# Optimization experiments

Measured on AMD Instinct MI355X. Metric: run time of the kernel, lower is better.

Reference implementation:

```python
import jax, jax.numpy as jnp
import numpy as np

B = 65536
QUERY_DIM = 1024
CROSS_DIM = 1024
HEADS = 16
DIM_HEAD = 64
INNER = HEADS * DIM_HEAD  # 1024
SCALE = DIM_HEAD ** -0.5


def setup_inputs() -> dict:
    key = jax.random.key(0)
    ks = jax.random.split(key, 7)
    s_in = 1.0 / np.sqrt(QUERY_DIM)
    s_c = 1.0 / np.sqrt(CROSS_DIM)
    s_o = 1.0 / np.sqrt(INNER)
    return {
        "latent": jax.random.normal(ks[0], (B, QUERY_DIM), jnp.float32),
        "cond_latent": jax.random.normal(ks[1], (B, CROSS_DIM), jnp.float32),
        "Wq": jax.random.normal(ks[2], (INNER, QUERY_DIM), jnp.float32) * s_in,
        "Wk": jax.random.normal(ks[3], (INNER, CROSS_DIM), jnp.float32) * s_c,
        "Wv": jax.random.normal(ks[4], (INNER, CROSS_DIM), jnp.float32) * s_c,
        "Wout": jax.random.normal(ks[5], (QUERY_DIM, INNER), jnp.float32) * s_o,
        "bout": jax.random.normal(ks[6], (QUERY_DIM,), jnp.float32) * s_o,
    }


def reference(latent, cond_latent, Wq, Wk, Wv, Wout, bout):
    # projections: [B, inner] -> [B, heads, dim_head]
    Q = (latent @ Wq.T).reshape(B, HEADS, DIM_HEAD)
    K = (cond_latent @ Wk.T).reshape(B, HEADS, DIM_HEAD)
    V = (cond_latent @ Wv.T).reshape(B, HEADS, DIM_HEAD)
    # attention across the heads axis: scores [B, heads, heads]
    scores = jnp.einsum("bhd,bgd->bhg", Q, K) * SCALE
    probs = jax.nn.softmax(scores, axis=-1)
    feats = jnp.einsum("bhg,bgd->bhd", probs, V).reshape(B, INNER)
    return feats @ Wout.T + bout
```

## Files before the change

kernel.cpp:

```cpp
#include <hip/hip_runtime.h>
#include <hip/hip_bf16.h>

#define NB    65536
#define KDIM  1024
#define NDIM  1024

#define BM 256
#define BN 256
#define BK 64
#define NT (KDIM / BK)

typedef float f32x4 __attribute__((ext_vector_type(4)));
typedef short short8 __attribute__((ext_vector_type(8)));
typedef unsigned short ushort8v __attribute__((ext_vector_type(8)));

static __device__ __forceinline__ unsigned short f2bf(float f) {
    union { float f; unsigned u; } v; v.f = f;
    unsigned r = v.u + 0x7FFFu + ((v.u >> 16) & 1u);
    return (unsigned short)(r >> 16);
}
static __device__ __forceinline__ float bf2f(unsigned short h) {
    union { unsigned u; float f; } v; v.u = ((unsigned)h) << 16;
    return v.f;
}

static __device__ __forceinline__ void gload16(const unsigned short* g, unsigned short* l) {
    __builtin_amdgcn_global_load_lds(
        (const __attribute__((address_space(1))) unsigned int*)g,
        (__attribute__((address_space(3))) unsigned int*)l, 16, 0, 0);
}

__global__ __launch_bounds__(256) void f32_to_bf16_k(
    const float* __restrict__ s, unsigned short* __restrict__ d, int n4)
{
    const int stride = gridDim.x * 256;
    for (int i = blockIdx.x * 256 + threadIdx.x; i < n4; i += stride) {
        float4 v = reinterpret_cast<const float4*>(s)[i];
        ushort4 o;
        o.x = f2bf(v.x); o.y = f2bf(v.y); o.z = f2bf(v.z); o.w = f2bf(v.w);
        reinterpret_cast<ushort4*>(d)[i] = o;
    }
}

template<int OUT_F32>
__global__ __launch_bounds__(512, 2) void gemm256(
    const unsigned short* __restrict__ Ap, const unsigned short* __restrict__ Wp,
    const float* __restrict__ bias, void* __restrict__ Cptr)
{
    constexpr int N = NDIM;
    constexpr int GN = NDIM / BN;
    __shared__ alignas(16) unsigned short lds[2][2][32][512];

    const int t    = threadIdx.x;
    const int lane = t & 63;
    const int wid  = t >> 6;
    const int wm   = wid >> 2;
    const int wn   = wid & 3;

    const int nwg  = gridDim.x;
    const int cpx  = nwg >> 3;
    const int orig = blockIdx.x;
    const int wgid = (orig & 7) * cpx + (orig >> 3);
    const int bn0  = (wgid & (GN - 1)) * BN;
    const int bm0  = (wgid / GN) * BM;

    const size_t aoff = (size_t)(lane & 15) * KDIM + (lane >> 4) * 8;

#define LDA_(BUF, MI, KS) \
    (*reinterpret_cast<const short8*>(&lds[BUF][0][(wm * 8 + (MI)) * 2 + (KS)][lane * 8]))
#define LDB_(BUF, NI, KS) \
    (*reinterpret_cast<const short8*>(&lds[BUF][1][(wn * 4 + (NI)) * 2 + (KS)][lane * 8]))

#define STAGE_(TAU, SLOT, AB, KS) do {                                          \
        int _tc = (TAU) < NT ? (TAU) : NT - 1;   \
        const unsigned short* _b = (AB) ? Wp : Ap;                              \
        int _r0 = (AB) ? bn0 : bm0;                                             \
        _Pragma("unroll")                                                       \
        for (int _j = 0; _j < 2; ++_j) {                                        \
            int _f = wid * 2 + _j;                                              \
            gload16(_b + (size_t)(_r0 + _f * 16) * KDIM + _tc * BK + (KS) * 32 + aoff, \
                    &lds[SLOT][AB][_f * 2 + (KS)][0]);                          \
        }                                                                       \
    } while (0)

#define PHASE_SYNC() do {                                                       \
        asm volatile("s_waitcnt vmcnt(8)" ::: "memory");                        \
        __builtin_amdgcn_s_barrier();                                           \
        asm volatile("s_waitcnt lgkmcnt(0)" ::: "memory");                      \
        __builtin_amdgcn_sched_barrier(0);                                      \
    } while (0)

#define MFMA_LO() do { _Pragma("unroll")                                        \
    for (int mi = 0; mi < 8; ++mi) {                                            \
        acc[mi][0] = __builtin_amdgcn_mfma_f32_16x16x32_bf16(af[mi], bq0, acc[mi][0], 0, 0, 0); \
        acc[mi][1] = __builtin_amdgcn_mfma_f32_16x16x32_bf16(af[mi], bq1, acc[mi][1], 0, 0, 0); \
    } } while (0)
#define MFMA_HI() do { _Pragma("unroll")                                        \
    for (int mi = 0; mi < 8; ++mi) {                                            \
        acc[mi][2] = __builtin_amdgcn_mfma_f32_16x16x32_bf16(af[mi], bq2, acc[mi][2], 0, 0, 0); \
        acc[mi][3] = __builtin_amdgcn_mfma_f32_16x16x32_bf16(af[mi], bq3, acc[mi][3], 0, 0, 0); \
    } } while (0)

#define GROUP_(BUF, OBUF, TT) do {                                              \
                                                      \
        _Pragma("unroll")                                                       \
        for (int mi = 0; mi < 8; ++mi) af[mi] = LDA_(BUF, mi, 0);               \
        bq0 = LDB_(BUF, 0, 0); bq1 = LDB_(BUF, 1, 0);                           \
        STAGE_((TT) + 1, OBUF, 0, 1);                                           \
        PHASE_SYNC();                                                           \
        __builtin_amdgcn_s_setprio(1); MFMA_LO(); __builtin_amdgcn_s_setprio(0);\
        __builtin_amdgcn_s_barrier();                                           \
                                                      \
        bq2 = LDB_(BUF, 2, 0); bq3 = LDB_(BUF, 3, 0);                           \
        STAGE_((TT) + 1, OBUF, 1, 1);                                           \
        PHASE_SYNC();                                                           \
        __builtin_amdgcn_s_setprio(1); MFMA_HI(); __builtin_amdgcn_s_setprio(0);\
        __builtin_amdgcn_s_barrier();                                           \
                                                      \
        _Pragma("unroll")                                                       \
        for (int mi = 0; mi < 8; ++mi) af[mi] = LDA_(BUF, mi, 1);               \
        bq0 = LDB_(BUF, 0, 1); bq1 = LDB_(BUF, 1, 1);                           \
        STAGE_((TT) + 2, BUF, 0, 0);                                            \
        PHASE_SYNC();                                                           \
        __builtin_amdgcn_s_setprio(1); MFMA_LO(); __builtin_amdgcn_s_setprio(0);\
        __builtin_amdgcn_s_barrier();                                           \
                                                      \
        bq2 = LDB_(BUF, 2, 1); bq3 = LDB_(BUF, 3, 1);                           \
        STAGE_((TT) + 2, BUF, 1, 0);                                            \
        PHASE_SYNC();                                                           \
        __builtin_amdgcn_s_setprio(1); MFMA_HI(); __builtin_amdgcn_s_setprio(0);\
        __builtin_amdgcn_s_barrier();                                           \
    } while (0)

    f32x4 acc[8][4];
#pragma unroll
    for (int mi = 0; mi < 8; ++mi)
#pragma unroll
        for (int ni = 0; ni < 4; ++ni)
            acc[mi][ni] = (f32x4){0.f, 0.f, 0.f, 0.f};

    short8 af[8], bq0, bq1, bq2, bq3;

    STAGE_(0, 0, 0, 0); STAGE_(0, 0, 1, 0);
    STAGE_(0, 0, 0, 1); STAGE_(0, 0, 1, 1);
    STAGE_(1, 1, 0, 0); STAGE_(1, 1, 1, 0);
    asm volatile("s_waitcnt vmcnt(8)" ::: "memory");
    __builtin_amdgcn_s_barrier();

#pragma unroll 1
    for (int tt = 0; tt < NT; tt += 2) {
        GROUP_(0, 1, tt);
        GROUP_(1, 0, tt + 1);
    }

    const int crow = (lane >> 4) * 4;
    const int ccol = lane & 15;
    if (OUT_F32) {
        float* Cf = (float*)Cptr;
        float bv[4];
#pragma unroll
        for (int ni = 0; ni < 4; ++ni)
            bv[ni] = bias[bn0 + wn * 64 + ni * 16 + ccol];
#pragma unroll
        for (int mi = 0; mi < 8; ++mi)
#pragma unroll
            for (int ni = 0; ni < 4; ++ni) {
                size_t base = (size_t)(bm0 + wm * 128 + mi * 16 + crow) * N
                            + (bn0 + wn * 64 + ni * 16 + ccol);
#pragma unroll
                for (int r = 0; r < 4; ++r)
                    Cf[base + (size_t)r * N] = acc[mi][ni][r] + bv[ni];
            }
    } else {
        unsigned short* Cb = (unsigned short*)Cptr;
#pragma unroll
        for (int mi = 0; mi < 8; ++mi)
#pragma unroll
            for (int ni = 0; ni < 4; ++ni) {
                size_t base = (size_t)(bm0 + wm * 128 + mi * 16 + crow) * N
                            + (bn0 + wn * 64 + ni * 16 + ccol);
#pragma unroll
                for (int r = 0; r < 4; ++r)
                    Cb[base + (size_t)r * N] = f2bf(acc[mi][ni][r]);
            }
    }
#undef LDA_
#undef LDB_
#undef STAGE_
#undef PHASE_SYNC
#undef MFMA_LO
#undef MFMA_HI
#undef GROUP_
}

__global__ __launch_bounds__(256) void attn_k(
    const unsigned short* __restrict__ Qb, const unsigned short* __restrict__ Kb,
    const unsigned short* __restrict__ Vb, unsigned short* __restrict__ Fb)
{
    __shared__ alignas(16) unsigned short KL[4][1024];
    __shared__ alignas(16) unsigned short VL[4][1024];
    const int t = threadIdx.x;
    const int lane = t & 63;
    const int wid = t >> 6;
    const size_t row = (size_t)blockIdx.x * 4 + wid;
    const size_t base = row * 1024;
    const int off = lane * 16;

    ushort8v q0 = *reinterpret_cast<const ushort8v*>(&Qb[base + off]);
    ushort8v q1 = *reinterpret_cast<const ushort8v*>(&Qb[base + off + 8]);
    float qf[16];
#pragma unroll
    for (int j = 0; j < 8; ++j) { qf[j] = bf2f(q0[j]); qf[8 + j] = bf2f(q1[j]); }

    *reinterpret_cast<ushort8v*>(&KL[wid][off])     = *reinterpret_cast<const ushort8v*>(&Kb[base + off]);
    *reinterpret_cast<ushort8v*>(&KL[wid][off + 8]) = *reinterpret_cast<const ushort8v*>(&Kb[base + off + 8]);
    *reinterpret_cast<ushort8v*>(&VL[wid][off])     = *reinterpret_cast<const ushort8v*>(&Vb[base + off]);
    *reinterpret_cast<ushort8v*>(&VL[wid][off + 8]) = *reinterpret_cast<const ushort8v*>(&Vb[base + off + 8]);
    __syncthreads();

    const int sub = lane & 3;
    float s[16];
#pragma unroll
    for (int g = 0; g < 16; ++g) {
        const ushort8v k0 = *reinterpret_cast<const ushort8v*>(&KL[wid][g * 64 + sub * 16]);
        const ushort8v k1 = *reinterpret_cast<const ushort8v*>(&KL[wid][g * 64 + sub * 16 + 8]);
        float acc = 0.f;
#pragma unroll
        for (int j = 0; j < 8; ++j)
            acc += qf[j] * bf2f(k0[j]) + qf[8 + j] * bf2f(k1[j]);
        s[g] = acc;
    }
#pragma unroll
    for (int m = 1; m <= 2; m <<= 1)
#pragma unroll
        for (int g = 0; g < 16; ++g)
            s[g] += __shfl_xor(s[g], m, 64);

    float mx = s[0];
#pragma unroll
    for (int g = 1; g < 16; ++g) mx = fmaxf(mx, s[g]);
    float p[16], denom = 0.f;
#pragma unroll
    for (int g = 0; g < 16; ++g) {
        p[g] = __expf((s[g] - mx) * 0.125f);
        denom += p[g];
    }
    float inv = 1.f / denom;

    float f[16];
#pragma unroll
    for (int j = 0; j < 16; ++j) f[j] = 0.f;
#pragma unroll
    for (int g = 0; g < 16; ++g) {
        float pg = p[g] * inv;
        const ushort8v v0 = *reinterpret_cast<const ushort8v*>(&VL[wid][g * 64 + sub * 16]);
        const ushort8v v1 = *reinterpret_cast<const ushort8v*>(&VL[wid][g * 64 + sub * 16 + 8]);
#pragma unroll
        for (int j = 0; j < 8; ++j) {
            f[j]     += pg * bf2f(v0[j]);
            f[8 + j] += pg * bf2f(v1[j]);
        }
    }
    ushort8v o0, o1;
#pragma unroll
    for (int j = 0; j < 8; ++j) { o0[j] = f2bf(f[j]); o1[j] = f2bf(f[8 + j]); }
    *reinterpret_cast<ushort8v*>(&Fb[base + off])     = o0;
    *reinterpret_cast<ushort8v*>(&Fb[base + off + 8]) = o1;
}

extern "C" void kernel_launch(void* const* d_in, const int* in_sizes, int n_in,
                              void* d_out, int out_size, void* d_ws, size_t ws_size,
                              hipStream_t stream)
{
    (void)in_sizes; (void)n_in; (void)out_size; (void)ws_size;
    const float* latent = (const float*)d_in[0];
    const float* cond   = (const float*)d_in[1];
    const float* Wq     = (const float*)d_in[2];
    const float* Wk     = (const float*)d_in[3];
    const float* Wv     = (const float*)d_in[4];
    const float* Wout   = (const float*)d_in[5];
    const float* bout   = (const float*)d_in[6];
    float* out = (float*)d_out;

    char* ws = (char*)d_ws;
    const size_t MB = 1ull << 20;
    unsigned short* wqb = (unsigned short*)(ws + 0 * MB);
    unsigned short* wkb = (unsigned short*)(ws + 2 * MB);
    unsigned short* wvb = (unsigned short*)(ws + 4 * MB);
    unsigned short* wob = (unsigned short*)(ws + 6 * MB);
    unsigned short* Qb  = (unsigned short*)(ws + 8 * MB);
    unsigned short* Kbf = (unsigned short*)(ws + 8 * MB + 128 * MB);
    unsigned short* Vbf = (unsigned short*)(ws + 8 * MB + 256 * MB);
    unsigned short* Lb  = (unsigned short*)(ws + 8 * MB + 384 * MB);
    unsigned short* Cb  = (unsigned short*)(ws + 8 * MB + 512 * MB);

    const int wn4 = (KDIM * NDIM) / 4;
    f32_to_bf16_k<<<1024, 256, 0, stream>>>(Wq,   wqb, wn4);
    f32_to_bf16_k<<<1024, 256, 0, stream>>>(Wk,   wkb, wn4);
    f32_to_bf16_k<<<1024, 256, 0, stream>>>(Wv,   wvb, wn4);
    f32_to_bf16_k<<<1024, 256, 0, stream>>>(Wout, wob, wn4);

    const int an4 = (NB * KDIM) / 4;
    f32_to_bf16_k<<<4096, 256, 0, stream>>>(latent, Lb, an4);
    f32_to_bf16_k<<<4096, 256, 0, stream>>>(cond,   Cb, an4);

    const int nblk = (NB / BM) * (NDIM / BN);
    gemm256<0><<<nblk, 512, 0, stream>>>(Lb, wqb, nullptr, Qb);
    gemm256<0><<<nblk, 512, 0, stream>>>(Cb, wkb, nullptr, Kbf);
    gemm256<0><<<nblk, 512, 0, stream>>>(Cb, wvb, nullptr, Vbf);

    attn_k<<<NB / 4, 256, 0, stream>>>(Qb, Kbf, Vbf, Qb);

    gemm256<1><<<nblk, 512, 0, stream>>>(Qb, wob, bout, out);
}
```

Measured before the change: 1.009 ms.

## Split GEMM phases by M-halves and relax per-phase memory waits

The bf16 GEMM inner loop now splits each k-slice into two M-halves, each covering all four N fragments, instead of splitting it into two N-halves covering all eight M fragments. B fragments are loaded once per k-slice. The explicit lgkmcnt(0) wait and the sched_barrier are dropped, and the vmcnt wait before the barrier now happens every other phase. The aim is to cut stall points and give the compiler more freedom to overlap LDS reads with MFMAs. In exchange, correctness now depends on the compiler-inserted waits and on fewer global-load waits being enough, and a final vmcnt(0) is added before the epilogue.

```diff
diff --git a/kernel.cpp b/kernel.cpp
--- a/kernel.cpp
+++ b/kernel.cpp
@@ -66,13 +66,18 @@
 
     const size_t aoff = (size_t)(lane & 15) * KDIM + (lane >> 4) * 8;
 
+#define FENCE_ asm volatile("" ::: "memory")
+#define BAR_   do { FENCE_; __builtin_amdgcn_s_barrier(); FENCE_; } while (0)
+#define VMBAR_ do { asm volatile("s_waitcnt vmcnt(8)" ::: "memory");            \
+                    __builtin_amdgcn_s_barrier(); FENCE_; } while (0)
+
 #define LDA_(BUF, MI, KS) \
     (*reinterpret_cast<const short8*>(&lds[BUF][0][(wm * 8 + (MI)) * 2 + (KS)][lane * 8]))
 #define LDB_(BUF, NI, KS) \
     (*reinterpret_cast<const short8*>(&lds[BUF][1][(wn * 4 + (NI)) * 2 + (KS)][lane * 8]))
 
 #define STAGE_(TAU, SLOT, AB, KS) do {                                          \
-        int _tc = (TAU) < NT ? (TAU) : NT - 1;   \
+        int _tc = (TAU) < NT ? (TAU) : NT - 1;    \
         const unsigned short* _b = (AB) ? Wp : Ap;                              \
         int _r0 = (AB) ? bn0 : bm0;                                             \
         _Pragma("unroll")                                                       \
@@ -83,53 +88,47 @@
         }                                                                       \
     } while (0)
 
-#define PHASE_SYNC() do {                                                       \
-        asm volatile("s_waitcnt vmcnt(8)" ::: "memory");                        \
-        __builtin_amdgcn_s_barrier();                                           \
-        asm volatile("s_waitcnt lgkmcnt(0)" ::: "memory");                      \
-        __builtin_amdgcn_sched_barrier(0);                                      \
-    } while (0)
-
-#define MFMA_LO() do { _Pragma("unroll")                                        \
-    for (int mi = 0; mi < 8; ++mi) {                                            \
-        acc[mi][0] = __builtin_amdgcn_mfma_f32_16x16x32_bf16(af[mi], bq0, acc[mi][0], 0, 0, 0); \
-        acc[mi][1] = __builtin_amdgcn_mfma_f32_16x16x32_bf16(af[mi], bq1, acc[mi][1], 0, 0, 0); \
+#define MFMA_(ACCB, AF) do { _Pragma("unroll")                                  \
+    for (int mi = 0; mi < 4; ++mi) {                                            \
+        acc[(ACCB) + mi][0] = __builtin_amdgcn_mfma_f32_16x16x32_bf16(AF[mi], bq0, acc[(ACCB) + mi][0], 0, 0, 0); \
+        acc[(ACCB) + mi][1] = __builtin_amdgcn_mfma_f32_16x16x32_bf16(AF[mi], bq1, acc[(ACCB) + mi][1], 0, 0, 0); \
+        acc[(ACCB) + mi][2] = __builtin_amdgcn_mfma_f32_16x16x32_bf16(AF[mi], bq2, acc[(ACCB) + mi][2], 0, 0, 0); \
+        acc[(ACCB) + mi][3] = __builtin_amdgcn_mfma_f32_16x16x32_bf16(AF[mi], bq3, acc[(ACCB) + mi][3], 0, 0, 0); \
     } } while (0)
-#define MFMA_HI() do { _Pragma("unroll")                                        \
-    for (int mi = 0; mi < 8; ++mi) {                                            \
-        acc[mi][2] = __builtin_amdgcn_mfma_f32_16x16x32_bf16(af[mi], bq2, acc[mi][2], 0, 0, 0); \
-        acc[mi][3] = __builtin_amdgcn_mfma_f32_16x16x32_bf16(af[mi], bq3, acc[mi][3], 0, 0, 0); \
-    } } while (0)
 
 #define GROUP_(BUF, OBUF, TT) do {                                              \
-                                                      \
-        _Pragma("unroll")                                                       \
-        for (int mi = 0; mi < 8; ++mi) af[mi] = LDA_(BUF, mi, 0);               \
+                                                   \
+        _Pragma("unroll")                                                       \
+        for (int mi = 0; mi < 4; ++mi) afA[mi] = LDA_(BUF, mi, 0);              \
         bq0 = LDB_(BUF, 0, 0); bq1 = LDB_(BUF, 1, 0);                           \
+        bq2 = LDB_(BUF, 2, 0); bq3 = LDB_(BUF, 3, 0);                           \
         STAGE_((TT) + 1, OBUF, 0, 1);                                           \
-        PHASE_SYNC();                                                           \
-        __builtin_amdgcn_s_setprio(1); MFMA_LO(); __builtin_amdgcn_s_setprio(0);\
-        __builtin_amdgcn_s_barrier();                                           \
-                                                      \
-        bq2 = LDB_(BUF, 2, 0); bq3 = LDB_(BUF, 3, 0);                           \
+        BAR_;                                                                   \
+        __builtin_amdgcn_s_setprio(1); MFMA_(0, afA); __builtin_amdgcn_s_setprio(0); \
+        BAR_;                                                                   \
+                                                   \
+        _Pragma("unroll")                                                       \
+        for (int mi = 0; mi < 4; ++mi) afB[mi] = LDA_(BUF, 4 + mi, 0);          \
         STAGE_((TT) + 1, OBUF, 1, 1);                                           \
-        PHASE_SYNC();                                                           \
-        __builtin_amdgcn_s_setprio(1); MFMA_HI(); __builtin_amdgcn_s_setprio(0);\
-        __builtin_amdgcn_s_barrier();                                           \
-                                                      \
-        _Pragma("unroll")                                                       \
-        for (int mi = 0; mi < 8; ++mi) af[mi] = LDA_(BUF, mi, 1);               \
+        VMBAR_;                                                                 \
+        __builtin_amdgcn_s_setprio(1); MFMA_(4, afB); __builtin_amdgcn_s_setprio(0); \
+        BAR_;                                                                   \
+                                                   \
+        _Pragma("unroll")                                                       \
+        for (int mi = 0; mi < 4; ++mi) afA[mi] = LDA_(BUF, mi, 1);              \
         bq0 = LDB_(BUF, 0, 1); bq1 = LDB_(BUF, 1, 1);                           \
+        bq2 = LDB_(BUF, 2, 1); bq3 = LDB_(BUF, 3, 1);                           \
         STAGE_((TT) + 2, BUF, 0, 0);                                            \
-        PHASE_SYNC();                                                           \
-        __builtin_amdgcn_s_setprio(1); MFMA_LO(); __builtin_amdgcn_s_setprio(0);\
-        __builtin_amdgcn_s_barrier();                                           \
-                                                      \
-        bq2 = LDB_(BUF, 2, 1); bq3 = LDB_(BUF, 3, 1);                           \
+        BAR_;                                                                   \
+        __builtin_amdgcn_s_setprio(1); MFMA_(0, afA); __builtin_amdgcn_s_setprio(0); \
+        BAR_;                                                                   \
+                                                   \
+        _Pragma("unroll")                                                       \
+        for (int mi = 0; mi < 4; ++mi) afB[mi] = LDA_(BUF, 4 + mi, 1);          \
         STAGE_((TT) + 2, BUF, 1, 0);                                            \
-        PHASE_SYNC();                                                           \
-        __builtin_amdgcn_s_setprio(1); MFMA_HI(); __builtin_amdgcn_s_setprio(0);\
-        __builtin_amdgcn_s_barrier();                                           \
+        VMBAR_;                                                                 \
+        __builtin_amdgcn_s_setprio(1); MFMA_(4, afB); __builtin_amdgcn_s_setprio(0); \
+        BAR_;                                                                   \
     } while (0)
 
     f32x4 acc[8][4];
@@ -139,19 +138,20 @@
         for (int ni = 0; ni < 4; ++ni)
             acc[mi][ni] = (f32x4){0.f, 0.f, 0.f, 0.f};
 
-    short8 af[8], bq0, bq1, bq2, bq3;
+    short8 afA[4], afB[4], bq0, bq1, bq2, bq3;
 
     STAGE_(0, 0, 0, 0); STAGE_(0, 0, 1, 0);
     STAGE_(0, 0, 0, 1); STAGE_(0, 0, 1, 1);
     STAGE_(1, 1, 0, 0); STAGE_(1, 1, 1, 0);
-    asm volatile("s_waitcnt vmcnt(8)" ::: "memory");
-    __builtin_amdgcn_s_barrier();
+    VMBAR_;
 
 #pragma unroll 1
     for (int tt = 0; tt < NT; tt += 2) {
         GROUP_(0, 1, tt);
         GROUP_(1, 0, tt + 1);
     }
+
+    asm volatile("s_waitcnt vmcnt(0)" ::: "memory");
 
     const int crow = (lane >> 4) * 4;
     const int ccol = lane & 15;
@@ -184,12 +184,13 @@
                     Cb[base + (size_t)r * N] = f2bf(acc[mi][ni][r]);
             }
     }
+#undef FENCE_
+#undef BAR_
+#undef VMBAR_
 #undef LDA_
 #undef LDB_
 #undef STAGE_
-#undef PHASE_SYNC
-#undef MFMA_LO
-#undef MFMA_HI
+#undef MFMA_
 #undef GROUP_
 }
 
```

Result: no change. 1.015 ms (+0.6%).
